# Kernel optimization log

Hardware: AMD Instinct MI355X
Metric: run time of the kernel (lower is better)

The kernel has to match this reference:

```python
import jax, jax.numpy as jnp
import numpy as np

NUM_HEADS = 8
ROPE_BASE = 10000.0


def _rope(x):
    # x: [b, n, c]; RoPE with channel_dims=(n,), feature_dim=c, k_max=c//2
    b, n, c = x.shape
    k_max = c // 2
    theta = 1.0 / (ROPE_BASE ** (jnp.arange(k_max, dtype=jnp.float32) / k_max))
    angles = jnp.arange(n, dtype=jnp.float32)[:, None] * theta  # [n, k_max]
    cos = jnp.cos(angles)
    sin = jnp.sin(angles)
    xr = x[..., 0::2]  # real parts  [b, n, k_max]
    xi = x[..., 1::2]  # imag parts
    pr = cos * xr - sin * xi
    pi = cos * xi + sin * xr
    # original concatenates real half then imag half (no re-interleave)
    return jnp.concatenate([pr, pi], axis=-1)


def setup_inputs() -> dict:
    key = jax.random.key(0)
    ks = jax.random.split(key, 5)
    b, n, c = 4, 4096, 1024
    x = jax.random.normal(ks[0], (b, n, c), dtype=jnp.float32)
    qk_w = jax.random.normal(ks[1], (c, 2 * c), dtype=jnp.float32) * (1.0 / np.sqrt(c))
    qk_b = jnp.zeros((2 * c,), dtype=jnp.float32)
    lepe_w = jax.random.normal(ks[2], (3, c, c), dtype=jnp.float32) * (1.0 / np.sqrt(3 * c))  # [W, I, O]
    lepe_b = jnp.zeros((c,), dtype=jnp.float32)
    return {"x": x, "qk_w": qk_w, "qk_b": qk_b, "lepe_w": lepe_w, "lepe_b": lepe_b}


def reference(x, qk_w, qk_b, lepe_w, lepe_b):
    b, n, c = x.shape
    h = NUM_HEADS
    d = c // h

    qk = x @ qk_w + qk_b
    q, k = jnp.split(qk, 2, axis=-1)
    q = jax.nn.elu(q) + 1.0
    k = jax.nn.elu(k) + 1.0

    q_rope = _rope(q)
    k_rope = _rope(k)

    def to_heads(t):  # [b, n, c] -> [b, h, n, d]
        return t.reshape(b, n, h, d).transpose(0, 2, 1, 3)

    qh = to_heads(q)
    kh = to_heads(k)
    qr = to_heads(q_rope)
    kr = to_heads(k_rope)
    vh = to_heads(x)

    # z = 1 / (q . mean_n(k) + eps)  -> [b, h, n, 1]
    k_mean = jnp.mean(kh, axis=2, keepdims=True)  # [b, h, 1, d]
    z = 1.0 / (jnp.einsum('bhnd,bhmd->bhnm', qh, k_mean) + 1e-6)

    # kv = k_rope^T v / sqrt(n)  -> [b, h, d, d]
    kv = jnp.einsum('bhnd,bhne->bhde', kr, vh) * (1.0 / jnp.sqrt(jnp.float32(n)))
    out = jnp.einsum('bhnd,bhde->bhne', qr, kv) * z  # [b, h, n, d]

    out = out.transpose(0, 2, 1, 3).reshape(b, n, c)

    # lepe: Conv1D(dim, 3, padding='same') applied to v (== original x)
    lepe = jax.lax.conv_general_dilated(
        x, lepe_w, window_strides=(1,), padding='SAME',
        dimension_numbers=('NWC', 'WIO', 'NWC')) + lepe_b
    return out + lepe
```

## Files before the change

### kernel.cpp

```cpp
#include <hip/hip_runtime.h>
#include <cmath>

#define BB 4
#define NN 4096
#define CC 1024
#define HH 8
#define DD 128
#define MM (BB*NN)
#define NP (NN+2)

typedef __attribute__((ext_vector_type(8))) short bf16x8;
typedef __attribute__((ext_vector_type(4))) float f32x4;

static __device__ __forceinline__ unsigned short f2bf(float f) {
    unsigned int u = __float_as_uint(f);
    unsigned int r = (u + 0x7FFF + ((u >> 16) & 1)) >> 16;
    return (unsigned short)r;
}
static __device__ __forceinline__ float bf2f(short s) {
    return __uint_as_float(((unsigned int)(unsigned short)s) << 16);
}
static __device__ __forceinline__ float4 bf4(ushort4 u) {
    float4 f;
    f.x = __uint_as_float((unsigned int)u.x << 16);
    f.y = __uint_as_float((unsigned int)u.y << 16);
    f.z = __uint_as_float((unsigned int)u.z << 16);
    f.w = __uint_as_float((unsigned int)u.w << 16);
    return f;
}

static __device__ __forceinline__ void load_lds16(const void* g, void* l) {
    __builtin_amdgcn_global_load_lds(
        (const __attribute__((address_space(1))) unsigned int*)g,
        (__attribute__((address_space(3))) unsigned int*)l, 16, 0, 0);
}

static __device__ __forceinline__ int swz(int row, int ko) {
    return (row * 64 + ko) ^ ((row & 7) << 3);
}

__global__ __launch_bounds__(256) void padx_kernel(
    const float* __restrict__ x, unsigned short* __restrict__ xpad)
{
    const int r = blockIdx.x;
    const int b = r / NP, p = r % NP;
    const int c = threadIdx.x * 4;
    ushort4 v = {0, 0, 0, 0};
    if (p >= 1 && p <= NN) {
        const float4 f = *(const float4*)&x[(size_t)(b * NN + p - 1) * CC + c];
        v.x = f2bf(f.x); v.y = f2bf(f.y); v.z = f2bf(f.z); v.w = f2bf(f.w);
    }
    *(ushort4*)&xpad[(size_t)r * CC + c] = v;
}

__global__ __launch_bounds__(256) void transpose_bf16_kernel(
    const float* __restrict__ src, unsigned short* __restrict__ dst,
    int R, int Cc)
{
    __shared__ float t[32][33];
    const int r0 = blockIdx.y * 32, c0 = blockIdx.x * 32;
    const int tx = threadIdx.x & 31, ty = threadIdx.x >> 5;
    #pragma unroll
    for (int i = 0; i < 4; ++i) {
        int r = ty + i * 8;
        t[r][tx] = src[(size_t)(r0 + r) * Cc + c0 + tx];
    }
    __syncthreads();
    #pragma unroll
    for (int i = 0; i < 4; ++i) {
        int r = ty + i * 8;
        dst[(size_t)(c0 + r) * R + r0 + tx] = f2bf(t[tx][r]);
    }
}

static __device__ __forceinline__ void stage_tile(
    const unsigned short* __restrict__ g, int stride,
    unsigned short* lds, int tid)
{
    const int wb = tid & ~63;
    #pragma unroll
    for (int l = 0; l < 4; ++l) {
        const int c = l * 512 + tid;
        const int row = c >> 3;
        const int col8 = (c & 7) ^ (row & 7);
        load_lds16(&g[(size_t)row * stride + col8 * 8],
                   &lds[(size_t)(l * 512 + wb) * 8]);
    }
}
static __device__ __forceinline__ void stage_ab(
    const unsigned short* __restrict__ Ag, int astride,
    const unsigned short* __restrict__ Bg, int bstride,
    unsigned short* As, unsigned short* Bs, int tid)
{
    stage_tile(Ag, astride, As, tid);
    stage_tile(Bg, bstride, Bs, tid);
}

__global__ __launch_bounds__(512) void gemm_qk_mfma(
    const unsigned short* __restrict__ xpad, const unsigned short* __restrict__ wT,
    const float* __restrict__ bias, unsigned short* __restrict__ qbuf,
    unsigned short* __restrict__ kbuf, float* __restrict__ ksum)
{
    __shared__ __align__(16) unsigned short As[2][16384];
    __shared__ __align__(16) unsigned short Bs[2][16384];
    const int m0 = blockIdx.x * 256;
    const int n0 = blockIdx.y * 256;
    const int tid = threadIdx.x;
    const int lane = tid & 63;
    const int wv = tid >> 6;
    const int wr = wv >> 2, wc = wv & 3;
    const int b = m0 >> 12;
    const int rbase = m0 + 1 + 2 * b;
    const int rl = lane & 15;

    f32x4 acc[8][4] = {};
    stage_ab(&xpad[(size_t)rbase * CC], CC, &wT[(size_t)n0 * CC], CC,
             As[0], Bs[0], tid);
    __syncthreads();
    for (int kt = 0; kt < 16; ++kt) {
        const int cur = kt & 1;
        if (kt + 1 < 16)
            stage_ab(&xpad[(size_t)rbase * CC + (kt + 1) * 64], CC,
                     &wT[(size_t)n0 * CC + (kt + 1) * 64], CC,
                     As[cur ^ 1], Bs[cur ^ 1], tid);
        const unsigned short* Ab = As[cur];
        const unsigned short* Bb = Bs[cur];
        #pragma unroll
        for (int ks = 0; ks < 2; ++ks) {
            const int ko = ks * 32 + (lane >> 4) * 8;
            bf16x8 af[8], bfr[4];
            #pragma unroll
            for (int mf = 0; mf < 8; ++mf)
                af[mf] = *(const bf16x8*)&Ab[swz(wr * 128 + mf * 16 + rl, ko)];
            #pragma unroll
            for (int nf = 0; nf < 4; ++nf)
                bfr[nf] = *(const bf16x8*)&Bb[swz(wc * 64 + nf * 16 + rl, ko)];
            #pragma unroll
            for (int mf = 0; mf < 8; ++mf)
                #pragma unroll
                for (int nf = 0; nf < 4; ++nf)
                    acc[mf][nf] = __builtin_amdgcn_mfma_f32_16x16x32_bf16(
                        af[mf], bfr[nf], acc[mf][nf], 0, 0, 0);
        }
        __syncthreads();
    }
    const bool khalf = (n0 >= CC);
    const int col = lane & 15, rb4 = (lane >> 4) * 4;
    #pragma unroll
    for (int nf = 0; nf < 4; ++nf) {
        const int n = n0 + wc * 64 + nf * 16 + col;
        const float bn = bias[n];
        float csum = 0.0f;
        #pragma unroll
        for (int mf = 0; mf < 8; ++mf)
            #pragma unroll
            for (int r = 0; r < 4; ++r) {
                const int m = m0 + wr * 128 + mf * 16 + rb4 + r;
                float v = acc[mf][nf][r] + bn;
                v = (v > 0.0f) ? (v + 1.0f) : expf(v);
                csum += v;
                if (!khalf) qbuf[(size_t)m * CC + n] = f2bf(v);
                else        kbuf[(size_t)m * CC + (n - CC)] = f2bf(v);
            }
        if (khalf) atomicAdd(&ksum[b * CC + (n - CC)], csum);
    }
}

__global__ __launch_bounds__(256) void rope_z_kernel(
    unsigned short* __restrict__ qbuf, const unsigned short* __restrict__ kbuf,
    const float* __restrict__ ksum, unsigned short* __restrict__ krP,
    float* __restrict__ zbuf)
{
    const int tid = threadIdx.x;
    const int row = tid >> 3;
    const int h = tid & 7;
    const int m = blockIdx.x * 32 + row;
    const int b = m >> 12;
    const int pos = m & (NN - 1);
    unsigned short* qrow = qbuf + (size_t)m * CC + h * DD;
    const unsigned short* krow = kbuf + (size_t)m * CC + h * DD;

    bf16x8 qv[16], kv8[16];
    #pragma unroll
    for (int i = 0; i < 16; ++i) {
        qv[i]  = *(const bf16x8*)&qrow[i * 8];
        kv8[i] = *(const bf16x8*)&krow[i * 8];
    }
    const float* km = ksum + b * CC + h * DD;
    float dot = 0.0f;
    #pragma unroll
    for (int i = 0; i < 16; ++i)
        #pragma unroll
        for (int jq = 0; jq < 8; ++jq)
            dot = fmaf(bf2f(qv[i][jq]), km[i * 8 + jq], dot);
    dot *= (1.0f / (float)NN);
    __syncthreads();
    zbuf[(size_t)m * HH + h] = 1.0f / (dot + 1e-6f);

    #pragma unroll
    for (int c8 = 0; c8 < 8; ++c8) {
        bf16x8 qpr, qpi, kpr, kpi;
        #pragma unroll
        for (int u = 0; u < 8; ++u) {
            const int jj = c8 * 8 + u;
            const int j = h * 64 + jj;
            const float theta = __builtin_exp2f((float)j * (-13.287712379549449f / 512.0f));
            float sv, cv;
            __sincosf((float)pos * theta, &sv, &cv);
            const int li = c8 * 2 + (u >> 2);
            const int le = (2 * u) & 7;
            const float q0 = bf2f(qv[li][le]),  q1 = bf2f(qv[li][le + 1]);
            const float k0 = bf2f(kv8[li][le]), k1 = bf2f(kv8[li][le + 1]);
            qpr[u] = (short)f2bf(cv * q0 - sv * q1);
            qpi[u] = (short)f2bf(cv * q1 + sv * q0);
            kpr[u] = (short)f2bf(cv * k0 - sv * k1);
            kpi[u] = (short)f2bf(cv * k1 + sv * k0);
        }
        *(bf16x8*)&qbuf[(size_t)m * CC + h * 64 + c8 * 8] = qpr;
        *(bf16x8*)&qbuf[(size_t)m * CC + 512 + h * 64 + c8 * 8] = qpi;
        unsigned short* kp1 = &krP[((size_t)(b * 8 + (h >> 1)) * NN + pos) * DD + (h & 1) * 64 + c8 * 8];
        unsigned short* kp2 = &krP[((size_t)(b * 8 + 4 + (h >> 1)) * NN + pos) * DD + (h & 1) * 64 + c8 * 8];
        *(bf16x8*)kp1 = kpr;
        *(bf16x8*)kp2 = kpi;
    }
}

__global__ __launch_bounds__(256) void kv_kernel(
    const unsigned short* __restrict__ krP, const unsigned short* __restrict__ xpad,
    float* __restrict__ kvpart)
{
    __shared__ float ksm[8][132];
    __shared__ float vsm[8][132];
    const int bh = blockIdx.x;
    const int slice = blockIdx.y;
    const int b = bh >> 3, h = bh & 7;
    const int n0 = slice * 256;
    const int tid = threadIdx.x;
    const int td = (tid >> 4) * 8;
    const int te = (tid & 15) * 8;
    const unsigned short* kp = krP + ((size_t)bh * NN + n0) * DD;
    const unsigned short* vp = xpad + ((size_t)(b * NP) + 1 + n0) * CC + h * DD;
    const int sr = tid >> 5;
    const int sc = (tid & 31) * 4;
    float acc[8][8] = {};
    ushort4 kq = *(const ushort4*)&kp[(size_t)sr * DD + sc];
    ushort4 vq = *(const ushort4*)&vp[(size_t)sr * CC + sc];
    for (int r0 = 0; r0 < 256; r0 += 8) {
        *(float4*)&ksm[sr][sc] = bf4(kq);
        *(float4*)&vsm[sr][sc] = bf4(vq);
        __syncthreads();
        if (r0 + 8 < 256) {
            kq = *(const ushort4*)&kp[(size_t)(r0 + 8 + sr) * DD + sc];
            vq = *(const ushort4*)&vp[(size_t)(r0 + 8 + sr) * CC + sc];
        }
        #pragma unroll
        for (int r = 0; r < 8; ++r) {
            float a[8], bv[8];
            *(float4*)&a[0]  = *(const float4*)&ksm[r][td];
            *(float4*)&a[4]  = *(const float4*)&ksm[r][td + 4];
            *(float4*)&bv[0] = *(const float4*)&vsm[r][te];
            *(float4*)&bv[4] = *(const float4*)&vsm[r][te + 4];
            #pragma unroll
            for (int i = 0; i < 8; ++i)
                #pragma unroll
                for (int j = 0; j < 8; ++j)
                    acc[i][j] = fmaf(a[i], bv[j], acc[i][j]);
        }
        __syncthreads();
    }
    float* op = kvpart + ((size_t)slice * 32 + bh) * (DD * DD);
    #pragma unroll
    for (int i = 0; i < 8; ++i)
        #pragma unroll
        for (int j = 0; j < 8; j += 4)
            *(float4*)&op[(td + i) * DD + te + j] = *(float4*)&acc[i][j];
}

__global__ __launch_bounds__(256) void kv_reduce_t_kernel(
    const float* __restrict__ kvpart, unsigned short* __restrict__ kvT)
{
    __shared__ float t[32][33];
    const int bh = blockIdx.y;
    const int dblk = blockIdx.x >> 2, eblk = blockIdx.x & 3;
    const int tx = threadIdx.x & 31, ty = threadIdx.x >> 5;
    #pragma unroll
    for (int i = 0; i < 4; ++i) {
        const int d = dblk * 32 + ty + i * 8;
        float s = 0.0f;
        #pragma unroll
        for (int sl = 0; sl < 16; ++sl)
            s += kvpart[((size_t)sl * 32 + bh) * (DD * DD) + (size_t)d * DD + eblk * 32 + tx];
        t[ty + i * 8][tx] = s * (1.0f / 64.0f);
    }
    __syncthreads();
    #pragma unroll
    for (int i = 0; i < 4; ++i) {
        const int e = ty + i * 8;
        kvT[((size_t)bh * DD + eblk * 32 + e) * DD + dblk * 32 + tx] = f2bf(t[tx][e]);
    }
}

__global__ __launch_bounds__(512) void lepe_mfma(
    const unsigned short* __restrict__ xpad, const unsigned short* __restrict__ wT,
    const float* __restrict__ bias, const unsigned short* __restrict__ qr,
    const unsigned short* __restrict__ kvT, const float* __restrict__ z,
    float* __restrict__ out)
{
    __shared__ __align__(16) unsigned short As[2][16384];
    __shared__ __align__(16) unsigned short Bs[2][16384];
    const int m0 = blockIdx.x * 256;
    const int n0 = blockIdx.y * 256;
    const int tid = threadIdx.x;
    const int lane = tid & 63;
    const int wv = tid >> 6;
    const int wr = wv >> 2, wc = wv & 3;
    const int b = m0 >> 12;
    const int rbase = m0 + 1 + 2 * b;
    const int rl = lane & 15;
    const int rb4 = (lane >> 4) * 4;
    const int h0 = n0 >> 7;
    const int hw = h0 + (wc >> 1);

    f32x4 acc[8][4] = {};

    #pragma unroll
    for (int kt = 0; kt < 2; ++kt) {
        stage_tile(&qr[(size_t)m0 * CC + h0 * DD + kt * 64], CC, As[0], tid);
        stage_tile(&qr[(size_t)m0 * CC + (h0 + 1) * DD + kt * 64], CC, As[1], tid);
        stage_tile(&kvT[(size_t)(b * 8 + h0) * DD * DD + kt * 64], DD, Bs[0], tid);
        __syncthreads();
        const unsigned short* Ab = As[wc >> 1];
        const unsigned short* Bb = Bs[0];
        #pragma unroll
        for (int ks = 0; ks < 2; ++ks) {
            const int ko = ks * 32 + (lane >> 4) * 8;
            bf16x8 af[8], bfr[4];
            #pragma unroll
            for (int mf = 0; mf < 8; ++mf)
                af[mf] = *(const bf16x8*)&Ab[swz(wr * 128 + mf * 16 + rl, ko)];
            #pragma unroll
            for (int nf = 0; nf < 4; ++nf)
                bfr[nf] = *(const bf16x8*)&Bb[swz(wc * 64 + nf * 16 + rl, ko)];
            #pragma unroll
            for (int mf = 0; mf < 8; ++mf)
                #pragma unroll
                for (int nf = 0; nf < 4; ++nf)
                    acc[mf][nf] = __builtin_amdgcn_mfma_f32_16x16x32_bf16(
                        af[mf], bfr[nf], acc[mf][nf], 0, 0, 0);
        }
        __syncthreads();
    }

    #pragma unroll
    for (int mf = 0; mf < 8; ++mf)
        #pragma unroll
        for (int r = 0; r < 4; ++r) {
            const float zz = z[(size_t)(m0 + wr * 128 + mf * 16 + rb4 + r) * HH + hw];
            #pragma unroll
            for (int nf = 0; nf < 4; ++nf)
                acc[mf][nf][r] *= zz;
        }

    stage_ab(&xpad[(size_t)(rbase - 1) * CC], CC, &wT[(size_t)n0 * (3 * CC)], 3 * CC,
             As[0], Bs[0], tid);
    __syncthreads();
    for (int kt = 0; kt < 48; ++kt) {
        const int cur = kt & 1;
        if (kt + 1 < 48) {
            const int k0n = (kt + 1) * 64;
            const int sh = (k0n >> 10) - 1;
            const int i0 = k0n & (CC - 1);
            stage_ab(&xpad[(size_t)(rbase + sh) * CC + i0], CC,
                     &wT[(size_t)n0 * (3 * CC) + k0n], 3 * CC,
                     As[cur ^ 1], Bs[cur ^ 1], tid);
        }
        const unsigned short* Ab = As[cur];
        const unsigned short* Bb = Bs[cur];
        #pragma unroll
        for (int ks = 0; ks < 2; ++ks) {
            const int ko = ks * 32 + (lane >> 4) * 8;
            bf16x8 af[8], bfr[4];
            #pragma unroll
            for (int mf = 0; mf < 8; ++mf)
                af[mf] = *(const bf16x8*)&Ab[swz(wr * 128 + mf * 16 + rl, ko)];
            #pragma unroll
            for (int nf = 0; nf < 4; ++nf)
                bfr[nf] = *(const bf16x8*)&Bb[swz(wc * 64 + nf * 16 + rl, ko)];
            #pragma unroll
            for (int mf = 0; mf < 8; ++mf)
                #pragma unroll
                for (int nf = 0; nf < 4; ++nf)
                    acc[mf][nf] = __builtin_amdgcn_mfma_f32_16x16x32_bf16(
                        af[mf], bfr[nf], acc[mf][nf], 0, 0, 0);
        }
        __syncthreads();
    }

    const int col = lane & 15;
    #pragma unroll
    for (int nf = 0; nf < 4; ++nf) {
        const int n = n0 + wc * 64 + nf * 16 + col;
        const float bn = bias[n];
        #pragma unroll
        for (int mf = 0; mf < 8; ++mf)
            #pragma unroll
            for (int r = 0; r < 4; ++r) {
                const int m = m0 + wr * 128 + mf * 16 + rb4 + r;
                out[(size_t)m * CC + n] = acc[mf][nf][r] + bn;
            }
    }
}

extern "C" void kernel_launch(void* const* d_in, const int* in_sizes, int n_in,
                              void* d_out, int out_size, void* d_ws, size_t ws_size,
                              hipStream_t stream)
{
    const float* x      = (const float*)d_in[0];
    const float* qk_w   = (const float*)d_in[1];
    const float* qk_b   = (const float*)d_in[2];
    const float* lepe_w = (const float*)d_in[3];
    const float* lepe_b = (const float*)d_in[4];
    float* out = (float*)d_out;

    float* ws     = (float*)d_ws;
    float* zbuf   = ws;
    float* ksum   = zbuf + (size_t)MM * HH;
    float* kvpart = ksum + (size_t)BB * CC;
    unsigned short* xpad = (unsigned short*)(kvpart + (size_t)16 * 32 * DD * DD);
    unsigned short* wqT  = xpad + (size_t)BB * NP * CC;
    unsigned short* wlT  = wqT + (size_t)2 * CC * CC;
    unsigned short* qbuf = wlT + (size_t)CC * 3 * CC;
    unsigned short* kbuf = qbuf + (size_t)MM * CC;
    unsigned short* krP  = kbuf + (size_t)MM * CC;
    unsigned short* kvT  = krP + (size_t)32 * NN * DD;

    hipMemsetAsync(ksum, 0, BB * CC * sizeof(float), stream);

    padx_kernel          <<<BB * NP,                      256, 0, stream>>>(x, xpad);
    transpose_bf16_kernel<<<dim3(2 * CC / 32, CC / 32),   256, 0, stream>>>(qk_w, wqT, CC, 2 * CC);
    transpose_bf16_kernel<<<dim3(CC / 32, 3 * CC / 32),   256, 0, stream>>>(lepe_w, wlT, 3 * CC, CC);

    gemm_qk_mfma      <<<dim3(MM / 256, 2048 / 256), 512, 0, stream>>>(xpad, wqT, qk_b, qbuf, kbuf, ksum);
    rope_z_kernel     <<<MM / 32,                    256, 0, stream>>>(qbuf, kbuf, ksum, krP, zbuf);
    kv_kernel         <<<dim3(32, 16),               256, 0, stream>>>(krP, xpad, kvpart);
    kv_reduce_t_kernel<<<dim3(16, 32),               256, 0, stream>>>(kvpart, kvT);
    lepe_mfma         <<<dim3(MM / 256, CC / 256),   512, 0, stream>>>(xpad, wlT, lepe_b, qbuf, kvT, zbuf, out);
}
```

Measured before the change: 519.1 us.

## Use partial vmcnt waits and raw barriers to overlap staging with MFMA

Replaces __syncthreads in the double-buffered GEMM loops of the QK and LePE kernels with explicit s_waitcnt vmcnt(8) plus s_barrier. The next tile's global-to-LDS loads can then stay in flight while the current tile is computed. It also raises wave priority around the MFMA block with s_setprio, factors the MFMA tile into a helper, and swaps expf for __expf in the ELU epilogue. The hand-counted vmcnt relies on each thread issuing exactly 8 loads per stage, so it is fragile if the load count or compiler scheduling changes.

```diff
diff --git a/kernel.cpp b/kernel.cpp
--- a/kernel.cpp
+++ b/kernel.cpp
@@ -39,6 +39,8 @@
     return (row * 64 + ko) ^ ((row & 7) << 3);
 }
 
+#define CFENCE() asm volatile("" ::: "memory")
+
 __global__ __launch_bounds__(256) void padx_kernel(
     const float* __restrict__ x, unsigned short* __restrict__ xpad)
 {
@@ -94,6 +96,32 @@
 {
     stage_tile(Ag, astride, As, tid);
     stage_tile(Bg, bstride, Bs, tid);
+}
+
+static __device__ __forceinline__ void mfma_tile(
+    const unsigned short* __restrict__ Ab, const unsigned short* __restrict__ Bb,
+    int wr, int wc, int lane, f32x4 acc[8][4])
+{
+    const int rl = lane & 15;
+    __builtin_amdgcn_s_setprio(1);
+    #pragma unroll
+    for (int ks = 0; ks < 2; ++ks) {
+        const int ko = ks * 32 + (lane >> 4) * 8;
+        bf16x8 af[8], bfr[4];
+        #pragma unroll
+        for (int mf = 0; mf < 8; ++mf)
+            af[mf] = *(const bf16x8*)&Ab[swz(wr * 128 + mf * 16 + rl, ko)];
+        #pragma unroll
+        for (int nf = 0; nf < 4; ++nf)
+            bfr[nf] = *(const bf16x8*)&Bb[swz(wc * 64 + nf * 16 + rl, ko)];
+        #pragma unroll
+        for (int mf = 0; mf < 8; ++mf)
+            #pragma unroll
+            for (int nf = 0; nf < 4; ++nf)
+                acc[mf][nf] = __builtin_amdgcn_mfma_f32_16x16x32_bf16(
+                    af[mf], bfr[nf], acc[mf][nf], 0, 0, 0);
+    }
+    __builtin_amdgcn_s_setprio(0);
 }
 
 __global__ __launch_bounds__(512) void gemm_qk_mfma(
@@ -111,38 +139,25 @@
     const int wr = wv >> 2, wc = wv & 3;
     const int b = m0 >> 12;
     const int rbase = m0 + 1 + 2 * b;
-    const int rl = lane & 15;
 
     f32x4 acc[8][4] = {};
     stage_ab(&xpad[(size_t)rbase * CC], CC, &wT[(size_t)n0 * CC], CC,
              As[0], Bs[0], tid);
-    __syncthreads();
     for (int kt = 0; kt < 16; ++kt) {
         const int cur = kt & 1;
-        if (kt + 1 < 16)
+        if (kt + 1 < 16) {
             stage_ab(&xpad[(size_t)rbase * CC + (kt + 1) * 64], CC,
                      &wT[(size_t)n0 * CC + (kt + 1) * 64], CC,
                      As[cur ^ 1], Bs[cur ^ 1], tid);
-        const unsigned short* Ab = As[cur];
-        const unsigned short* Bb = Bs[cur];
-        #pragma unroll
-        for (int ks = 0; ks < 2; ++ks) {
-            const int ko = ks * 32 + (lane >> 4) * 8;
-            bf16x8 af[8], bfr[4];
-            #pragma unroll
-            for (int mf = 0; mf < 8; ++mf)
-                af[mf] = *(const bf16x8*)&Ab[swz(wr * 128 + mf * 16 + rl, ko)];
-            #pragma unroll
-            for (int nf = 0; nf < 4; ++nf)
-                bfr[nf] = *(const bf16x8*)&Bb[swz(wc * 64 + nf * 16 + rl, ko)];
-            #pragma unroll
-            for (int mf = 0; mf < 8; ++mf)
-                #pragma unroll
-                for (int nf = 0; nf < 4; ++nf)
-                    acc[mf][nf] = __builtin_amdgcn_mfma_f32_16x16x32_bf16(
-                        af[mf], bfr[nf], acc[mf][nf], 0, 0, 0);
-        }
-        __syncthreads();
+            asm volatile("s_waitcnt vmcnt(8)" ::: "memory");
+        } else {
+            asm volatile("s_waitcnt vmcnt(0)" ::: "memory");
+        }
+        __builtin_amdgcn_s_barrier();
+        CFENCE();
+        mfma_tile(As[cur], Bs[cur], wr, wc, lane, acc);
+        CFENCE();
+        __builtin_amdgcn_s_barrier();
     }
     const bool khalf = (n0 >= CC);
     const int col = lane & 15, rb4 = (lane >> 4) * 4;
@@ -157,7 +172,7 @@
             for (int r = 0; r < 4; ++r) {
                 const int m = m0 + wr * 128 + mf * 16 + rb4 + r;
                 float v = acc[mf][nf][r] + bn;
-                v = (v > 0.0f) ? (v + 1.0f) : expf(v);
+                v = (v > 0.0f) ? (v + 1.0f) : __expf(v);
                 csum += v;
                 if (!khalf) qbuf[(size_t)m * CC + n] = f2bf(v);
                 else        kbuf[(size_t)m * CC + (n - CC)] = f2bf(v);
@@ -316,7 +331,6 @@
     const int wr = wv >> 2, wc = wv & 3;
     const int b = m0 >> 12;
     const int rbase = m0 + 1 + 2 * b;
-    const int rl = lane & 15;
     const int rb4 = (lane >> 4) * 4;
     const int h0 = n0 >> 7;
     const int hw = h0 + (wc >> 1);
@@ -329,25 +343,7 @@
         stage_tile(&qr[(size_t)m0 * CC + (h0 + 1) * DD + kt * 64], CC, As[1], tid);
         stage_tile(&kvT[(size_t)(b * 8 + h0) * DD * DD + kt * 64], DD, Bs[0], tid);
         __syncthreads();
-        const unsigned short* Ab = As[wc >> 1];
-        const unsigned short* Bb = Bs[0];
-        #pragma unroll
-        for (int ks = 0; ks < 2; ++ks) {
-            const int ko = ks * 32 + (lane >> 4) * 8;
-            bf16x8 af[8], bfr[4];
-            #pragma unroll
-            for (int mf = 0; mf < 8; ++mf)
-                af[mf] = *(const bf16x8*)&Ab[swz(wr * 128 + mf * 16 + rl, ko)];
-            #pragma unroll
-            for (int nf = 0; nf < 4; ++nf)
-                bfr[nf] = *(const bf16x8*)&Bb[swz(wc * 64 + nf * 16 + rl, ko)];
-            #pragma unroll
-            for (int mf = 0; mf < 8; ++mf)
-                #pragma unroll
-                for (int nf = 0; nf < 4; ++nf)
-                    acc[mf][nf] = __builtin_amdgcn_mfma_f32_16x16x32_bf16(
-                        af[mf], bfr[nf], acc[mf][nf], 0, 0, 0);
-        }
+        mfma_tile(As[wc >> 1], Bs[0], wr, wc, lane, acc);
         __syncthreads();
     }
 
@@ -360,10 +356,10 @@
             for (int nf = 0; nf < 4; ++nf)
                 acc[mf][nf][r] *= zz;
         }
+    asm volatile("s_waitcnt vmcnt(0)" ::: "memory");
 
     stage_ab(&xpad[(size_t)(rbase - 1) * CC], CC, &wT[(size_t)n0 * (3 * CC)], 3 * CC,
              As[0], Bs[0], tid);
-    __syncthreads();
     for (int kt = 0; kt < 48; ++kt) {
         const int cur = kt & 1;
         if (kt + 1 < 48) {
@@ -373,27 +369,15 @@
             stage_ab(&xpad[(size_t)(rbase + sh) * CC + i0], CC,
                      &wT[(size_t)n0 * (3 * CC) + k0n], 3 * CC,
                      As[cur ^ 1], Bs[cur ^ 1], tid);
-        }
-        const unsigned short* Ab = As[cur];
-        const unsigned short* Bb = Bs[cur];
-        #pragma unroll
-        for (int ks = 0; ks < 2; ++ks) {
-            const int ko = ks * 32 + (lane >> 4) * 8;
-            bf16x8 af[8], bfr[4];
-            #pragma unroll
-            for (int mf = 0; mf < 8; ++mf)
-                af[mf] = *(const bf16x8*)&Ab[swz(wr * 128 + mf * 16 + rl, ko)];
-            #pragma unroll
-            for (int nf = 0; nf < 4; ++nf)
-                bfr[nf] = *(const bf16x8*)&Bb[swz(wc * 64 + nf * 16 + rl, ko)];
-            #pragma unroll
-            for (int mf = 0; mf < 8; ++mf)
-                #pragma unroll
-                for (int nf = 0; nf < 4; ++nf)
-                    acc[mf][nf] = __builtin_amdgcn_mfma_f32_16x16x32_bf16(
-                        af[mf], bfr[nf], acc[mf][nf], 0, 0, 0);
-        }
-        __syncthreads();
+            asm volatile("s_waitcnt vmcnt(8)" ::: "memory");
+        } else {
+            asm volatile("s_waitcnt vmcnt(0)" ::: "memory");
+        }
+        __builtin_amdgcn_s_barrier();
+        CFENCE();
+        mfma_tile(As[cur], Bs[cur], wr, wc, lane, acc);
+        CFENCE();
+        __builtin_amdgcn_s_barrier();
     }
 
     const int col = lane & 15;
```

Result: no change. 510.5 us (-1.7%).
